# Performance work log

Measured on AMD Instinct MI355X. Metric: run time of the kernel, lower is better.

The kernel has to match this reference:

```python
import jax, jax.numpy as jnp
import numpy as np

E, D, H, T = 8, 2048, 5632, 32768  # experts, dim, hidden_dim, total routed tokens


def setup_inputs() -> dict:
    key = jax.random.key(0)
    k_x, k1, k2, k3 = jax.random.split(key, 4)
    x = jax.random.normal(k_x, (T, D), dtype=jnp.float32)
    # trunc_normal init stds per init_weights (approx: plain normal, same scale)
    std = (2.0 / (D * 24)) ** 0.5
    w1 = jax.random.normal(k1, (E, H, D), dtype=jnp.float32) * std
    w2 = jax.random.normal(k2, (E, D, H), dtype=jnp.float32) * std
    w3 = jax.random.normal(k3, (E, H, D), dtype=jnp.float32) * std
    # tokens are pre-sorted by expert; even split 4096 tokens/expert (sums to T)
    num_tokens_per_expert = jnp.full((E,), T // E, dtype=jnp.int32)
    return {"x": x, "w1": w1, "w2": w2, "w3": w3,
            "num_tokens_per_expert": num_tokens_per_expert}


def _grouped_experts(x, w1, w2, w3, counts):
    # Faithful to _run_experts_grouped_mm: grouped GEMMs computed in bf16,
    # SwiGLU activation, cast back to x dtype.
    xb = x.astype(jnp.bfloat16)
    w1b = jnp.transpose(w1.astype(jnp.bfloat16), (0, 2, 1))  # [E, D, H]
    w3b = jnp.transpose(w3.astype(jnp.bfloat16), (0, 2, 1))  # [E, D, H]
    w2b = jnp.transpose(w2.astype(jnp.bfloat16), (0, 2, 1))  # [E, H, D]
    h1 = jax.lax.ragged_dot(xb, w1b, counts)   # [T, H]
    h3 = jax.lax.ragged_dot(xb, w3b, counts)   # [T, H]
    h = jax.nn.silu(h1) * h3                   # fused SwiGLU gate
    out = jax.lax.ragged_dot(h, w2b, counts)   # [T, D]
    return out.astype(x.dtype)


def reference(x, w1, w2, w3, num_tokens_per_expert):
    return _grouped_experts(x, w1, w2, w3, num_tokens_per_expert)
```

## Files before the change

kernel.cpp:

```cpp
#include <hip/hip_runtime.h>
#include <hip/hip_bf16.h>
#include <stdint.h>

#define TT 32768
#define DD 2048
#define HH 5632
#define NE 8

typedef __bf16 bf16;
typedef __bf16 bf16x8 __attribute__((ext_vector_type(8)));
typedef float  f32x4  __attribute__((ext_vector_type(4)));

__device__ __forceinline__ void gl16(const void* g, void* l) {
    __builtin_amdgcn_global_load_lds(
        (const __attribute__((address_space(1))) void*)g,
        (__attribute__((address_space(3))) void*)l, 16, 0, 0);
}
#define VMW(n) asm volatile("s_waitcnt vmcnt(" #n ")" ::: "memory")
#define LGKM0() do { asm volatile("s_waitcnt lgkmcnt(0)" ::: "memory"); \
                     __builtin_amdgcn_sched_barrier(0); } while (0)
#define BARRIER() __builtin_amdgcn_s_barrier()

__device__ __forceinline__ int swz(int off) { return off ^ (((off >> 7) & 3) << 4); }

__device__ __forceinline__ int expert_of(const int* counts, int row0) {
    int base = 0;
    for (int i = 0; i < NE; ++i) { int c = counts[i]; if (row0 < base + c) return i; base += c; }
    return NE - 1;
}

__global__ __launch_bounds__(256)
void k_cvt(const float* __restrict__ in, bf16* __restrict__ out, long n) {
    long i = ((long)blockIdx.x * 256 + threadIdx.x) * 8;
    const long stride = (long)gridDim.x * 256 * 8;
    for (; i < n; i += stride) {
        const float4* p = (const float4*)(in + i);
        float4 a = p[0], b = p[1];
        union { bf16 v[8]; uint4 u; } r;
        r.v[0] = (bf16)a.x; r.v[1] = (bf16)a.y; r.v[2] = (bf16)a.z; r.v[3] = (bf16)a.w;
        r.v[4] = (bf16)b.x; r.v[5] = (bf16)b.y; r.v[6] = (bf16)b.z; r.v[7] = (bf16)b.w;
        *(uint4*)(out + i) = r.u;
    }
}

#define M1_LOAD(bufb, NA, NB1, NB3) do {                                      \
    const char* nb_ = sm + (bufb);                                            \
    _Pragma("unroll")                                                         \
    for (int mi = 0; mi < 8; ++mi)                                            \
        NA[mi] = *(const bf16x8*)(nb_ + aoff0 + mi * 1024);                   \
    _Pragma("unroll")                                                         \
    for (int ni = 0; ni < 2; ++ni) {                                          \
        NB1[ni] = *(const bf16x8*)(nb_ + 16384 + boff0 + ni * 1024);          \
        NB3[ni] = *(const bf16x8*)(nb_ + 24576 + boff0 + ni * 1024);          \
    }                                                                         \
    __builtin_amdgcn_sched_barrier(0);                                        \
} while (0)

#define M1_ITER(g, bLb, bSb, ko, CA, CB1, CB3, NA, NB1, NB3) do {             \
    if ((g) + 4 < GTOT) { stage((ko), (bSb)); VMW(8); }                       \
    else if ((g) == GTOT - 4) { VMW(4); }                                     \
    else if ((g) == GTOT - 3) { VMW(0); }                                     \
    LGKM0();                                                                  \
    if ((g) + 1 < GTOT) M1_LOAD((bLb), NA, NB1, NB3);                         \
    __builtin_amdgcn_s_setprio(1);                                            \
    _Pragma("unroll")                                                         \
    for (int mi = 0; mi < 8; ++mi)                                            \
    _Pragma("unroll")                                                         \
    for (int ni = 0; ni < 2; ++ni) {                                          \
        acc1[mi][ni] = __builtin_amdgcn_mfma_f32_16x16x32_bf16(CA[mi], CB1[ni], acc1[mi][ni], 0, 0, 0); \
        acc3[mi][ni] = __builtin_amdgcn_mfma_f32_16x16x32_bf16(CA[mi], CB3[ni], acc3[mi][ni], 0, 0, 0); \
    }                                                                         \
    __builtin_amdgcn_s_setprio(0);                                            \
    BARRIER();                                                                \
} while (0)

__global__ __launch_bounds__(512, 2)
void k_moe1(const bf16* __restrict__ xb, const bf16* __restrict__ w1b,
            const bf16* __restrict__ w3b, const int* __restrict__ counts,
            bf16* __restrict__ h) {
    extern __shared__ __align__(16) char sm[];
    const int tid = threadIdx.x;
    const int c = blockIdx.x & 7;
    const int j = blockIdx.x >> 3;
    const int NSEG = 22;
    const int NT = 64;
    const int GTOT = NSEG * NT;

    const int s0 = swz(tid * 16);
    const int s1 = 8192 + s0;
    const int dst0 = tid * 16;

    const char *sa0, *sa1, *sa2, *sa3;
    int sseg = 0;
    auto set_bases = [&](int sg) {
        int local = sg * 32 + j;
        int r0 = ((c << 4) + (local & 15)) * 256;
        int c0 = (local >> 4) * 128;
        int e = expert_of(counts, r0);
        sa0 = (const char*)xb + (((size_t)(r0 + (s0 >> 6)) * DD) << 1) + (s0 & 63);
        sa1 = (const char*)xb + (((size_t)(r0 + (s1 >> 6)) * DD) << 1) + (s1 & 63);
        const char* w1p = (const char*)(w1b + (size_t)e * HH * DD);
        const char* w3p = (const char*)(w3b + (size_t)e * HH * DD);
        sa2 = w1p + (((size_t)(c0 + (s0 >> 6)) * DD) << 1) + (s0 & 63);
        sa3 = w3p + (((size_t)(c0 + (s0 >> 6)) * DD) << 1) + (s0 & 63);
    };
    set_bases(0);

    auto stage = [&](int ko, int bufb) {
        char* db = sm + bufb;
        gl16(sa0 + ko, db + dst0);
        gl16(sa1 + ko, db + 8192 + dst0);
        gl16(sa2 + ko, db + 16384 + dst0);
        gl16(sa3 + ko, db + 24576 + dst0);
    };

    const int lane = tid & 63, wv = tid >> 6;
    const int wrow = wv >> 2, wcol = wv & 3;
    const int lrow = lane & 15, kb = (lane >> 4) << 4;
    const int aoff0 = swz((wrow * 128 + lrow) * 64 + kb);
    const int boff0 = swz((wcol * 32 + lrow) * 64 + kb);

    f32x4 acc1[8][2] = {};
    f32x4 acc3[8][2] = {};
    bf16x8 Xa[8], Xb1[2], Xb3[2], Ya[8], Yb1[2], Yb3[2];

    stage(0, 0); stage(64, 32768); stage(128, 65536); stage(192, 98304);
    VMW(8);
    BARRIER();
    M1_LOAD(0, Xa, Xb1, Xb3);

    int tc = 0;
    int stk = 256;
    int b0 = 0;
    int cseg = 0;
    int crow0 = ((c << 4) + (j & 15)) * 256;
    int ccol0 = (j >> 4) * 128;

    for (int gp = 0; gp < GTOT; gp += 2) {
        int bL1 = b0 + 1; if (bL1 >= 5) bL1 -= 5;
        int bL2 = b0 + 2; if (bL2 >= 5) bL2 -= 5;
        int bS1 = b0 + 4; if (bS1 >= 5) bS1 -= 5;
        const int bS2 = b0;
        if (tc == 60 && sseg + 1 < NSEG) { ++sseg; set_bases(sseg); stk = 0; }

        M1_ITER(gp,     bL1 << 15, bS1 << 15, stk,      Xa, Xb1, Xb3, Ya, Yb1, Yb3);
        M1_ITER(gp + 1, bL2 << 15, bS2 << 15, stk + 64, Ya, Yb1, Yb3, Xa, Xb1, Xb3);
        stk += 128;
        b0 += 2; if (b0 >= 5) b0 -= 5;

        if (tc == 62) {
#pragma unroll
            for (int mi = 0; mi < 8; ++mi)
#pragma unroll
                for (int ni = 0; ni < 2; ++ni) {
#pragma unroll
                    for (int jj = 0; jj < 4; ++jj) {
                        int row = crow0 + wrow * 128 + mi * 16 + ((lane >> 4) << 2) + jj;
                        int col = ccol0 + wcol * 32 + ni * 16 + lrow;
                        float f1 = (float)(bf16)acc1[mi][ni][jj];
                        float f3 = (float)(bf16)acc3[mi][ni][jj];
                        float s = f1 / (1.0f + __expf(-f1));
                        h[(size_t)row * HH + col] = (bf16)(s * f3);
                    }
                    acc1[mi][ni] = (f32x4){0.f, 0.f, 0.f, 0.f};
                    acc3[mi][ni] = (f32x4){0.f, 0.f, 0.f, 0.f};
                }
            ++cseg;
            int local = cseg * 32 + j;
            crow0 = ((c << 4) + (local & 15)) * 256;
            ccol0 = (local >> 4) * 128;
            tc = 0;
        } else {
            tc += 2;
        }
    }
}

#define G2_LOAD(bufb, NA, NB) do {                                            \
    const char* nb_ = sm + (bufb);                                            \
    _Pragma("unroll")                                                         \
    for (int mi = 0; mi < 8; ++mi)                                            \
        NA[mi] = *(const bf16x8*)(nb_ + aoff0 + mi * 1024);                   \
    _Pragma("unroll")                                                         \
    for (int ni = 0; ni < 4; ++ni)                                            \
        NB[ni] = *(const bf16x8*)(nb_ + 16384 + boff0 + ni * 1024);           \
    __builtin_amdgcn_sched_barrier(0);                                        \
} while (0)

#define G2_ITER(g, bLb, bSb, ko, CA, CB, NA, NB) do {                         \
    if ((g) + 4 < GTOT) { stage((ko), (bSb)); VMW(8); }                       \
    else if ((g) == GTOT - 4) { VMW(4); }                                     \
    else if ((g) == GTOT - 3) { VMW(0); }                                     \
    LGKM0();                                                                  \
    if ((g) + 1 < GTOT) G2_LOAD((bLb), NA, NB);                               \
    __builtin_amdgcn_s_setprio(1);                                            \
    _Pragma("unroll")                                                         \
    for (int mi = 0; mi < 8; ++mi)                                            \
    _Pragma("unroll")                                                         \
    for (int ni = 0; ni < 4; ++ni)                                            \
        acc[mi][ni] = __builtin_amdgcn_mfma_f32_16x16x32_bf16(CA[mi], CB[ni], acc[mi][ni], 0, 0, 0); \
    __builtin_amdgcn_s_setprio(0);                                            \
    BARRIER();                                                                \
} while (0)

__global__ __launch_bounds__(512, 2)
void k_g2(const bf16* __restrict__ hb, const bf16* __restrict__ w2b,
          const int* __restrict__ counts, float* __restrict__ out) {
    extern __shared__ __align__(16) char sm[];
    const int tid = threadIdx.x;
    const int c = blockIdx.x & 7;
    const int j = blockIdx.x >> 3;
    const int NSEG = 4;
    const int NT = 176;
    const int GTOT = NSEG * NT;

    const int s0 = swz(tid * 16);
    const int s1 = 8192 + s0;
    const int dst0 = tid * 16;

    const char *sa0, *sa1, *sa2, *sa3;
    int sseg = 0;
    auto set_bases = [&](int sg) {
        int local = sg * 32 + j;
        int r0 = ((c << 4) + (local & 15)) * 256;
        int c0 = (local >> 4) * 256;
        int e = expert_of(counts, r0);
        sa0 = (const char*)hb + (((size_t)(r0 + (s0 >> 6)) * HH) << 1) + (s0 & 63);
        sa1 = (const char*)hb + (((size_t)(r0 + (s1 >> 6)) * HH) << 1) + (s1 & 63);
        const char* wp = (const char*)(w2b + (size_t)e * DD * HH);
        sa2 = wp + (((size_t)(c0 + (s0 >> 6)) * HH) << 1) + (s0 & 63);
        sa3 = wp + (((size_t)(c0 + (s1 >> 6)) * HH) << 1) + (s1 & 63);
    };
    set_bases(0);

    auto stage = [&](int ko, int bufb) {
        char* db = sm + bufb;
        gl16(sa0 + ko, db + dst0);
        gl16(sa1 + ko, db + 8192 + dst0);
        gl16(sa2 + ko, db + 16384 + dst0);
        gl16(sa3 + ko, db + 24576 + dst0);
    };

    const int lane = tid & 63, wv = tid >> 6;
    const int wrow = wv >> 2, wcol = wv & 3;
    const int lrow = lane & 15, kb = (lane >> 4) << 4;
    const int aoff0 = swz((wrow * 128 + lrow) * 64 + kb);
    const int boff0 = swz((wcol * 64 + lrow) * 64 + kb);

    f32x4 acc[8][4] = {};
    bf16x8 Xa[8], Xb[4], Ya[8], Yb[4];

    stage(0, 0); stage(64, 32768); stage(128, 65536); stage(192, 98304);
    VMW(8);
    BARRIER();
    G2_LOAD(0, Xa, Xb);

    int tc = 0, stk = 256, b0 = 0;
    int cseg = 0;
    int crow0 = ((c << 4) + (j & 15)) * 256;
    int ccol0 = (j >> 4) * 256;

    for (int gp = 0; gp < GTOT; gp += 2) {
        int bL1 = b0 + 1; if (bL1 >= 5) bL1 -= 5;
        int bL2 = b0 + 2; if (bL2 >= 5) bL2 -= 5;
        int bS1 = b0 + 4; if (bS1 >= 5) bS1 -= 5;
        const int bS2 = b0;
        if (tc == 172 && sseg + 1 < NSEG) { ++sseg; set_bases(sseg); stk = 0; }

        G2_ITER(gp,     bL1 << 15, bS1 << 15, stk,      Xa, Xb, Ya, Yb);
        G2_ITER(gp + 1, bL2 << 15, bS2 << 15, stk + 64, Ya, Yb, Xa, Xb);
        stk += 128;
        b0 += 2; if (b0 >= 5) b0 -= 5;

        if (tc == 174) {
#pragma unroll
            for (int mi = 0; mi < 8; ++mi)
#pragma unroll
                for (int ni = 0; ni < 4; ++ni) {
#pragma unroll
                    for (int jj = 0; jj < 4; ++jj) {
                        int row = crow0 + wrow * 128 + mi * 16 + ((lane >> 4) << 2) + jj;
                        int col = ccol0 + wcol * 64 + ni * 16 + lrow;
                        out[(size_t)row * DD + col] = (float)(bf16)acc[mi][ni][jj];
                    }
                    acc[mi][ni] = (f32x4){0.f, 0.f, 0.f, 0.f};
                }
            ++cseg;
            int local = cseg * 32 + j;
            crow0 = ((c << 4) + (local & 15)) * 256;
            ccol0 = (local >> 4) * 256;
            tc = 0;
        } else {
            tc += 2;
        }
    }
}

extern "C" void kernel_launch(void* const* d_in, const int* in_sizes, int n_in,
                              void* d_out, int out_size, void* d_ws, size_t ws_size,
                              hipStream_t stream) {
    const float* x      = (const float*)d_in[0];
    const float* w1     = (const float*)d_in[1];
    const float* w2     = (const float*)d_in[2];
    const float* w3     = (const float*)d_in[3];
    const int*   counts = (const int*)d_in[4];
    float* out = (float*)d_out;

    const size_t xb_b = (size_t)TT * DD * 2;
    const size_t h_b  = (size_t)TT * HH * 2;
    const size_t w_b  = (size_t)NE * HH * DD * 2;
    const size_t need_full = xb_b + h_b + 2 * w_b;
    if (ws_size < need_full) return;

    bf16* xb  = (bf16*)d_ws;
    bf16* h   = (bf16*)((char*)d_ws + xb_b);
    bf16* wsA = (bf16*)((char*)d_ws + xb_b + h_b);
    bf16* wsB = (bf16*)((char*)d_ws + xb_b + h_b + w_b);

    hipFuncSetAttribute((const void*)k_moe1, hipFuncAttributeMaxDynamicSharedMemorySize, 163840);
    hipFuncSetAttribute((const void*)k_g2,   hipFuncAttributeMaxDynamicSharedMemorySize, 163840);

    k_cvt<<<2048, 256, 0, stream>>>(x,  xb,  (long)TT * DD);
    k_cvt<<<2048, 256, 0, stream>>>(w1, wsA, (long)NE * HH * DD);
    k_cvt<<<2048, 256, 0, stream>>>(w3, wsB, (long)NE * HH * DD);
    k_moe1<<<256, 512, 163840, stream>>>(xb, wsA, wsB, counts, h);
    k_cvt<<<2048, 256, 0, stream>>>(w2, wsA, (long)NE * DD * HH);
    k_g2<<<256, 512, 163840, stream>>>(h, wsA, counts, out);
}
```

Measured before the change: 3.174 ms.

## Replace persistent multi-tile k_g2 loop with one output tile per block

The second grouped GEMM kernel no longer runs 256 persistent blocks that each walk four output tiles while carrying the load pipeline across tile boundaries. It now launches 1024 blocks, each computing one 256x256 output tile over the full hidden dimension and then writing the result. This removes the segment and buffer-index bookkeeping inside the hot loop and lets the hardware scheduler balance tiles. The cost is a pipeline fill and drain per tile and extra block launch overhead, since with 160KB of LDS only one block fits per CU.

```diff
diff --git a/kernel.cpp b/kernel.cpp
--- a/kernel.cpp
+++ b/kernel.cpp
@@ -129,9 +129,7 @@
     BARRIER();
     M1_LOAD(0, Xa, Xb1, Xb3);
 
-    int tc = 0;
-    int stk = 256;
-    int b0 = 0;
+    int tc = 0, stk = 256, b0 = 0;
     int cseg = 0;
     int crow0 = ((c << 4) + (j & 15)) * 256;
     int ccol0 = (j >> 4) * 128;
@@ -176,8 +174,8 @@
     }
 }
 
-#define G2_LOAD(bufb, NA, NB) do {                                            \
-    const char* nb_ = sm + (bufb);                                            \
+#define G2_LOAD(t1, NA, NB) do {                                              \
+    const char* nb_ = sm + (size_t)((t1) % 5) * 32768;                        \
     _Pragma("unroll")                                                         \
     for (int mi = 0; mi < 8; ++mi)                                            \
         NA[mi] = *(const bf16x8*)(nb_ + aoff0 + mi * 1024);                   \
@@ -187,12 +185,12 @@
     __builtin_amdgcn_sched_barrier(0);                                        \
 } while (0)
 
-#define G2_ITER(g, bLb, bSb, ko, CA, CB, NA, NB) do {                         \
-    if ((g) + 4 < GTOT) { stage((ko), (bSb)); VMW(8); }                       \
-    else if ((g) == GTOT - 4) { VMW(4); }                                     \
-    else if ((g) == GTOT - 3) { VMW(0); }                                     \
+#define G2_ITER(t, CA, CB, NA, NB) do {                                       \
+    if ((t) + 4 < NT) { stage((t) + 4); VMW(8); }                             \
+    else if ((t) == NT - 4) { VMW(4); }                                       \
+    else if ((t) == NT - 3) { VMW(0); }                                       \
     LGKM0();                                                                  \
-    if ((g) + 1 < GTOT) G2_LOAD((bLb), NA, NB);                               \
+    if ((t) + 1 < NT) G2_LOAD((t) + 1, NA, NB);                               \
     __builtin_amdgcn_s_setprio(1);                                            \
     _Pragma("unroll")                                                         \
     for (int mi = 0; mi < 8; ++mi)                                            \
@@ -209,32 +207,26 @@
     extern __shared__ __align__(16) char sm[];
     const int tid = threadIdx.x;
     const int c = blockIdx.x & 7;
-    const int j = blockIdx.x >> 3;
-    const int NSEG = 4;
-    const int NT = 176;
-    const int GTOT = NSEG * NT;
-
-    const int s0 = swz(tid * 16);
-    const int s1 = 8192 + s0;
+    const int local = blockIdx.x >> 3;
+    const int nt = local >> 4;
+    const int mt = (c << 4) + (local & 15);
+    const int row0 = mt * 256, col0 = nt * 256;
+    const int e = expert_of(counts, row0);
+
+    const char *sa0, *sa1, *sa2, *sa3;
+    {
+        int off0 = tid * 16, off1 = 8192 + tid * 16;
+        int s0 = swz(off0), s1 = swz(off1);
+        sa0 = (const char*)hb + (((size_t)(row0 + (s0 >> 6)) * HH) << 1) + (s0 & 63);
+        sa1 = (const char*)hb + (((size_t)(row0 + (s1 >> 6)) * HH) << 1) + (s1 & 63);
+        const char* wp = (const char*)(w2b + (size_t)e * DD * HH);
+        sa2 = wp + (((size_t)(col0 + (s0 >> 6)) * HH) << 1) + (s0 & 63);
+        sa3 = wp + (((size_t)(col0 + (s1 >> 6)) * HH) << 1) + (s1 & 63);
+    }
     const int dst0 = tid * 16;
-
-    const char *sa0, *sa1, *sa2, *sa3;
-    int sseg = 0;
-    auto set_bases = [&](int sg) {
-        int local = sg * 32 + j;
-        int r0 = ((c << 4) + (local & 15)) * 256;
-        int c0 = (local >> 4) * 256;
-        int e = expert_of(counts, r0);
-        sa0 = (const char*)hb + (((size_t)(r0 + (s0 >> 6)) * HH) << 1) + (s0 & 63);
-        sa1 = (const char*)hb + (((size_t)(r0 + (s1 >> 6)) * HH) << 1) + (s1 & 63);
-        const char* wp = (const char*)(w2b + (size_t)e * DD * HH);
-        sa2 = wp + (((size_t)(c0 + (s0 >> 6)) * HH) << 1) + (s0 & 63);
-        sa3 = wp + (((size_t)(c0 + (s1 >> 6)) * HH) << 1) + (s1 & 63);
-    };
-    set_bases(0);
-
-    auto stage = [&](int ko, int bufb) {
-        char* db = sm + bufb;
+    auto stage = [&](int kt) {
+        char* db = sm + (size_t)(kt % 5) * 32768;
+        const size_t ko = (size_t)kt << 6;
         gl16(sa0 + ko, db + dst0);
         gl16(sa1 + ko, db + 8192 + dst0);
         gl16(sa2 + ko, db + 16384 + dst0);
@@ -244,56 +236,33 @@
     const int lane = tid & 63, wv = tid >> 6;
     const int wrow = wv >> 2, wcol = wv & 3;
     const int lrow = lane & 15, kb = (lane >> 4) << 4;
+
     const int aoff0 = swz((wrow * 128 + lrow) * 64 + kb);
     const int boff0 = swz((wcol * 64 + lrow) * 64 + kb);
 
     f32x4 acc[8][4] = {};
     bf16x8 Xa[8], Xb[4], Ya[8], Yb[4];
 
-    stage(0, 0); stage(64, 32768); stage(128, 65536); stage(192, 98304);
+    const int NT = HH / 32;
+    stage(0); stage(1); stage(2); stage(3);
     VMW(8);
     BARRIER();
     G2_LOAD(0, Xa, Xb);
-
-    int tc = 0, stk = 256, b0 = 0;
-    int cseg = 0;
-    int crow0 = ((c << 4) + (j & 15)) * 256;
-    int ccol0 = (j >> 4) * 256;
-
-    for (int gp = 0; gp < GTOT; gp += 2) {
-        int bL1 = b0 + 1; if (bL1 >= 5) bL1 -= 5;
-        int bL2 = b0 + 2; if (bL2 >= 5) bL2 -= 5;
-        int bS1 = b0 + 4; if (bS1 >= 5) bS1 -= 5;
-        const int bS2 = b0;
-        if (tc == 172 && sseg + 1 < NSEG) { ++sseg; set_bases(sseg); stk = 0; }
-
-        G2_ITER(gp,     bL1 << 15, bS1 << 15, stk,      Xa, Xb, Ya, Yb);
-        G2_ITER(gp + 1, bL2 << 15, bS2 << 15, stk + 64, Ya, Yb, Xa, Xb);
-        stk += 128;
-        b0 += 2; if (b0 >= 5) b0 -= 5;
-
-        if (tc == 174) {
-#pragma unroll
-            for (int mi = 0; mi < 8; ++mi)
-#pragma unroll
-                for (int ni = 0; ni < 4; ++ni) {
-#pragma unroll
-                    for (int jj = 0; jj < 4; ++jj) {
-                        int row = crow0 + wrow * 128 + mi * 16 + ((lane >> 4) << 2) + jj;
-                        int col = ccol0 + wcol * 64 + ni * 16 + lrow;
-                        out[(size_t)row * DD + col] = (float)(bf16)acc[mi][ni][jj];
-                    }
-                    acc[mi][ni] = (f32x4){0.f, 0.f, 0.f, 0.f};
-                }
-            ++cseg;
-            int local = cseg * 32 + j;
-            crow0 = ((c << 4) + (local & 15)) * 256;
-            ccol0 = (local >> 4) * 256;
-            tc = 0;
-        } else {
-            tc += 2;
-        }
-    }
+    for (int t = 0; t < NT; t += 2) {
+        G2_ITER(t,     Xa, Xb, Ya, Yb);
+        G2_ITER(t + 1, Ya, Yb, Xa, Xb);
+    }
+
+#pragma unroll
+    for (int mi = 0; mi < 8; ++mi)
+#pragma unroll
+        for (int ni = 0; ni < 4; ++ni)
+#pragma unroll
+            for (int j = 0; j < 4; ++j) {
+                int row = row0 + wrow * 128 + mi * 16 + ((lane >> 4) << 2) + j;
+                int col = col0 + wcol * 64 + ni * 16 + lrow;
+                out[(size_t)row * DD + col] = (float)(bf16)acc[mi][ni][j];
+            }
 }
 
 extern "C" void kernel_launch(void* const* d_in, const int* in_sizes, int n_in,
@@ -325,5 +294,5 @@
     k_cvt<<<2048, 256, 0, stream>>>(w3, wsB, (long)NE * HH * DD);
     k_moe1<<<256, 512, 163840, stream>>>(xb, wsA, wsB, counts, h);
     k_cvt<<<2048, 256, 0, stream>>>(w2, wsA, (long)NE * DD * HH);
-    k_g2<<<256, 512, 163840, stream>>>(h, wsA, counts, out);
-}
+    k_g2<<<1024, 512, 163840, stream>>>(h, wsA, counts, out);
+}
```

Result: faster. 2.648 ms (-16.6%).
